# Performance work log

Measured on AMD Instinct MI355X. Metric: run time of the kernel, lower is better.

Reference implementation:

```python
import jax, jax.numpy as jnp
import numpy as np

DIM = 1024
N_HEADS = 16
HEAD_DIM = DIM // N_HEADS
BATCH = 2
SEQ = 2048


def rotate_half(x):
    x1, x2 = jnp.split(x, 2, axis=-1)
    return jnp.concatenate((-x2, x1), axis=-1)


def rope_cos_sin(seq_len, head_dim, dtype=jnp.float32):
    inv_freq = 1.0 / (10000.0 ** (jnp.arange(0, head_dim, 2, dtype=jnp.float32) / head_dim))
    t = jnp.arange(seq_len, dtype=jnp.float32)
    freqs = jnp.einsum('i,j->ij', t, inv_freq)          # [S, hd/2]
    emb = jnp.concatenate((freqs, freqs), axis=-1)       # [S, hd]
    return emb.astype(dtype)[None, :, None, :]           # [1, S, 1, hd] (cos/sin applied below)


def setup_inputs() -> dict:
    key = jax.random.key(0)
    k_x, k_q, k_k, k_v, k_o = jax.random.split(key, 5)
    scale = 1.0 / np.sqrt(DIM)
    x = jax.random.normal(k_x, (BATCH, SEQ, DIM), dtype=jnp.float32)
    Wq = jax.random.normal(k_q, (DIM, DIM), dtype=jnp.float32) * scale
    Wk = jax.random.normal(k_k, (DIM, DIM), dtype=jnp.float32) * scale
    Wv = jax.random.normal(k_v, (DIM, DIM), dtype=jnp.float32) * scale
    Wo = jax.random.normal(k_o, (DIM, DIM), dtype=jnp.float32) * scale
    # causal mask: scores masked where mask == 0
    mask = jnp.tril(jnp.ones((SEQ, SEQ), dtype=jnp.int32))[None, None, :, :]
    return {"x": x, "Wq": Wq, "Wk": Wk, "Wv": Wv, "Wo": Wo, "mask": mask}


def reference(x, Wq, Wk, Wv, Wo, mask):
    B, S, _ = x.shape
    # torch nn.Linear: y = x @ W.T
    q = (x @ Wq.T).reshape(B, S, N_HEADS, HEAD_DIM)
    k = (x @ Wk.T).reshape(B, S, N_HEADS, HEAD_DIM)
    v = (x @ Wv.T).reshape(B, S, N_HEADS, HEAD_DIM)
    ang = rope_cos_sin(S, HEAD_DIM, x.dtype)
    cos, sin = jnp.cos(ang), jnp.sin(ang)
    q = q * cos + rotate_half(q) * sin
    k = k * cos + rotate_half(k) * sin
    # [B, H, S, hd]
    q = q.transpose(0, 2, 1, 3)
    k = k.transpose(0, 2, 1, 3)
    v = v.transpose(0, 2, 1, 3)
    scores = jnp.einsum('bhqd,bhkd->bhqk', q, k) / np.sqrt(HEAD_DIM)
    scores = jnp.where(mask == 0, jnp.asarray(-1e9, scores.dtype), scores)
    attn = jax.nn.softmax(scores, axis=-1)
    out = jnp.einsum('bhqk,bhkd->bhqd', attn, v)
    out = out.transpose(0, 2, 1, 3).reshape(B, S, DIM)
    return out @ Wo.T
```

## Files before the change

### kernel.cpp

```cpp
#include <hip/hip_runtime.h>
#include <stdint.h>

typedef unsigned short u16;
typedef __bf16 bf16x8 __attribute__((ext_vector_type(8)));
typedef __bf16 bf16x4 __attribute__((ext_vector_type(4)));
typedef float f32x4 __attribute__((ext_vector_type(4)));

#define N_B 2
#define N_S 2048
#define N_D 1024
#define N_H 16
#define HD 64

#if __has_builtin(__builtin_amdgcn_exp2f)
#define EXP2F(x) __builtin_amdgcn_exp2f(x)
#else
#define EXP2F(x) exp2f(x)
#endif

__device__ __forceinline__ u16 f2bf(float f) {
  union { float f; uint32_t u; } v; v.f = f;
  uint32_t u = v.u + 0x7fffu + ((v.u >> 16) & 1u);
  return (u16)(u >> 16);
}

__device__ __forceinline__ void gload16(const u16* g, u16* lds) {
  __builtin_amdgcn_global_load_lds(
      (const __attribute__((address_space(1))) unsigned int*)g,
      (__attribute__((address_space(3))) unsigned int*)lds, 16, 0, 0);
}

__global__ __launch_bounds__(256) void prep_kernel(
    const float* __restrict__ x, const float* __restrict__ Wq,
    const float* __restrict__ Wk, const float* __restrict__ Wv,
    const float* __restrict__ Wo,
    u16* __restrict__ xb, u16* __restrict__ wqb, u16* __restrict__ wkb,
    u16* __restrict__ wvb, u16* __restrict__ wob,
    float* __restrict__ cosT, float* __restrict__ sinT)
{
  const int NX = N_B * N_S * N_D;
  const int NW = N_D * N_D;
  int bid = blockIdx.x;
  if (bid < 8192) {
    int i = (bid * 256 + threadIdx.x) * 4;
    const float* src; u16* dst; int off;
    if (i < NX) { src = x; dst = xb; off = i; }
    else {
      int j = i - NX;
      int w = j >> 20;
      off = j & (NW - 1);
      src = (w == 0) ? Wq : (w == 1) ? Wk : (w == 2) ? Wv : Wo;
      dst = (w == 0) ? wqb : (w == 1) ? wkb : (w == 2) ? wvb : wob;
    }
    float4 v = *(const float4*)(src + off);
    ushort4 o;
    o.x = f2bf(v.x); o.y = f2bf(v.y); o.z = f2bf(v.z); o.w = f2bf(v.w);
    *(ushort4*)(dst + off) = o;
  } else {
    int t = (bid - 8192) * 256 + threadIdx.x;
    int s = t >> 5, i = t & 31;
    float inv = expf(-(float)i * 0.28782313662425574f);
    float a = (float)s * inv;
    float sn, cs;
    sincosf(a, &sn, &cs);
    cosT[t] = cs;
    sinT[t] = sn;
  }
}

__global__ __launch_bounds__(256, 5) void proj_kernel(
    const u16* __restrict__ x, const u16* __restrict__ Wq,
    const u16* __restrict__ Wk, const u16* __restrict__ Wv,
    u16* __restrict__ Qb, u16* __restrict__ Kb, u16* __restrict__ Vtb,
    const float* __restrict__ cosT, const float* __restrict__ sinT)
{
  const int mode = blockIdx.z;
  const u16* Wm = (mode == 0) ? Wq : (mode == 1) ? Wk : Wv;
  const int bx = blockIdx.x, by = blockIdx.y;
  const int tid = threadIdx.x;
  const int wave = tid >> 6, lane = tid & 63;
  const int c = lane & 15, quad = lane >> 4;

  __shared__ __align__(16) u16 As[128 * 64];
  __shared__ __align__(16) u16 Bs[64 * 64];

  const f32x4 zero = {0.f, 0.f, 0.f, 0.f};
  f32x4 acc[2][4];
#pragma unroll
  for (int i = 0; i < 2; ++i)
#pragma unroll
    for (int j = 0; j < 4; ++j) acc[i][j] = zero;

  for (int kt = 0; kt < 16; ++kt) {
    const int k0 = kt * 64;
    __syncthreads();
#pragma unroll
    for (int t = 0; t < 4; ++t) {
      int p = t * 256 + tid;
      int m = p >> 3, sl = p & 7;
      int kq = sl ^ (m & 7);
      gload16(x + (size_t)(by * 128 + m) * N_D + k0 + kq * 8, &As[(t * 256 + wave * 64) * 8]);
    }
#pragma unroll
    for (int t = 0; t < 2; ++t) {
      int p = t * 256 + tid;
      int m = p >> 3, sl = p & 7;
      int kq = sl ^ (m & 7);
      gload16(Wm + (size_t)(bx * 64 + m) * N_D + k0 + kq * 8, &Bs[(t * 256 + wave * 64) * 8]);
    }
    __syncthreads();
#pragma unroll
    for (int ks = 0; ks < 2; ++ks) {
      bf16x8 av[2], bv[4];
      int kq = ks * 4 + quad;
#pragma unroll
      for (int i = 0; i < 2; ++i) {
        int m = wave * 32 + i * 16 + c;
        av[i] = *(const bf16x8*)&As[(m * 8 + (kq ^ (m & 7))) * 8];
      }
#pragma unroll
      for (int j = 0; j < 4; ++j) {
        int n = j * 16 + c;
        bv[j] = *(const bf16x8*)&Bs[(n * 8 + (kq ^ (n & 7))) * 8];
      }
#pragma unroll
      for (int i = 0; i < 2; ++i)
#pragma unroll
        for (int j = 0; j < 4; ++j)
          acc[i][j] = __builtin_amdgcn_mfma_f32_16x16x32_bf16(av[i], bv[j], acc[i][j], 0, 0, 0);
    }
  }

  const int h = bx;
  if (mode < 2) {
    u16* Out = (mode == 0) ? Qb : Kb;
#pragma unroll
    for (int i = 0; i < 2; ++i) {
#pragma unroll
      for (int r = 0; r < 4; ++r) {
        int row = by * 128 + wave * 32 + i * 16 + quad * 4 + r;
        int b = row >> 11, s = row & 2047;
        float cs0 = cosT[s * 32 + c],      sn0 = sinT[s * 32 + c];
        float cs1 = cosT[s * 32 + 16 + c], sn1 = sinT[s * 32 + 16 + c];
        size_t base = ((size_t)(b * N_H + h) * N_S + s) * HD;
#pragma unroll
        for (int j = 0; j < 4; ++j) {
          float v = acc[i][j][r];
          float p = acc[i][j ^ 2][r];
          float cs = (j & 1) ? cs1 : cs0;
          float sn = (j & 1) ? sn1 : sn0;
          float res = (j < 2) ? (v * cs - p * sn) : (v * cs + p * sn);
          Out[base + j * 16 + c] = f2bf(res);
        }
      }
    }
  } else {
#pragma unroll
    for (int i = 0; i < 2; ++i) {
      int srow = by * 128 + wave * 32 + i * 16 + quad * 4;
      int b = srow >> 11, sb = srow & 2047;
#pragma unroll
      for (int j = 0; j < 4; ++j) {
        int d = j * 16 + c;
        ushort4 pk;
        pk.x = f2bf(acc[i][j][0]);
        pk.y = f2bf(acc[i][j][1]);
        pk.z = f2bf(acc[i][j][2]);
        pk.w = f2bf(acc[i][j][3]);
        *(ushort4*)&Vtb[((size_t)(b * N_H + h) * HD + d) * N_S + sb] = pk;
      }
    }
  }
}

__global__ __launch_bounds__(64, 2) void attn_kernel(
    const u16* __restrict__ Qb, const u16* __restrict__ Kb,
    const u16* __restrict__ Vtb, u16* __restrict__ Ab)
{
  const int lane = threadIdx.x;
  const int c = lane & 15, quad = lane >> 4;
  const int bx = blockIdx.x;
  const int xcd = bx & 7;
  const int idx = bx >> 3;
  const int t = 63 - (idx >> 2);
  const int bh = xcd + (idx & 3) * 8;
  const int q0 = t * 32;
  const int ktmax = t >> 1;
  const int maskch = t & 1;

  __shared__ __align__(16) u16 Ks[2][64 * 64];
  __shared__ __align__(16) u16 Ps[32 * 32];

  const u16* Qg = Qb + ((size_t)bh * N_S + q0) * HD;
  const u16* Kg = Kb + (size_t)bh * N_S * HD;
  const u16* Vg = Vtb + (size_t)bh * HD * N_S;

  bf16x8 qreg[2][2];
#pragma unroll
  for (int jQ = 0; jQ < 2; ++jQ)
#pragma unroll
    for (int ks = 0; ks < 2; ++ks)
      qreg[jQ][ks] = *(const bf16x8*)(Qg + (jQ * 16 + c) * HD + ks * 32 + quad * 8);

  const f32x4 zero = {0.f, 0.f, 0.f, 0.f};
  f32x4 acc_o[2][4];
#pragma unroll
  for (int mt = 0; mt < 2; ++mt)
#pragma unroll
    for (int nt = 0; nt < 4; ++nt) acc_o[mt][nt] = zero;
  float lrow[2] = {0.f, 0.f};

  const float CLOG = 0.18033688011112042f;
  const float FM = 16.0f;

#pragma unroll
  for (int i = 0; i < 8; ++i) {
    int ci = i * 64 + lane;
    int m = ci >> 3, sl = ci & 7;
    int kq = sl ^ (m & 7);
    gload16(Kg + (size_t)m * HD + kq * 8, &Ks[0][i * 512]);
  }
  asm volatile("" ::: "memory");
  bf16x8 vf[2][4];
#pragma unroll
  for (int ch = 0; ch < 2; ++ch)
#pragma unroll
    for (int nt = 0; nt < 4; ++nt)
      vf[ch][nt] = *(const bf16x8*)(Vg + (size_t)(nt * 16 + c) * N_S + ch * 32 + quad * 8);

  for (int kt = 0; kt <= ktmax; ++kt) {
    const u16* kb = &Ks[kt & 1][0];
    if (kt < ktmax) {
#pragma unroll
      for (int i = 0; i < 8; ++i) {
        int ci = i * 64 + lane;
        int m = ci >> 3, sl = ci & 7;
        int kq = sl ^ (m & 7);
        gload16(Kg + (size_t)((kt + 1) * 64 + m) * HD + kq * 8, &Ks[(kt + 1) & 1][i * 512]);
      }
      asm volatile("s_waitcnt vmcnt(16)" ::: "memory");
    } else {
      asm volatile("s_waitcnt vmcnt(8)" ::: "memory");
    }

    const bool diag = (kt == ktmax);
    const int nch = (diag && maskch == 0) ? 1 : 2;

#pragma unroll
    for (int ch = 0; ch < 2; ++ch) {
      if (ch < nch) {
        f32x4 acc_s[2][2];
#pragma unroll
        for (int iK = 0; iK < 2; ++iK)
#pragma unroll
          for (int jQ = 0; jQ < 2; ++jQ) acc_s[iK][jQ] = zero;
#pragma unroll
        for (int ks = 0; ks < 2; ++ks) {
          bf16x8 kf[2];
          int kq = ks * 4 + quad;
#pragma unroll
          for (int iK = 0; iK < 2; ++iK) {
            int m = ch * 32 + iK * 16 + c;
            kf[iK] = *(const bf16x8*)&kb[(m * 8 + (kq ^ (m & 7))) * 8];
          }
#pragma unroll
          for (int iK = 0; iK < 2; ++iK)
#pragma unroll
            for (int jQ = 0; jQ < 2; ++jQ)
              acc_s[iK][jQ] = __builtin_amdgcn_mfma_f32_16x16x32_bf16(
                  kf[iK], qreg[jQ][ks], acc_s[iK][jQ], 0, 0, 0);
        }

        const bool domask = diag && (ch == maskch);
#pragma unroll
        for (int iK = 0; iK < 2; ++iK)
#pragma unroll
          for (int jQ = 0; jQ < 2; ++jQ) {
            bf16x4 pb;
#pragma unroll
            for (int rr = 0; rr < 4; ++rr) {
              float arg = fmaf(acc_s[iK][jQ][rr], CLOG, -FM);
              if (domask) {
                int dsk = iK * 16 + quad * 4 + rr;
                int dq = jQ * 16 + c;
                if (dsk > dq) arg = -3.0e38f;
              }
              float p = EXP2F(arg);
              lrow[jQ] += p;
              pb[rr] = (__bf16)p;
            }
            int q = jQ * 16 + c;
            int slot = (iK * 2 + (quad >> 1)) ^ (q & 3);
            *(bf16x4*)&Ps[q * 32 + slot * 8 + (quad & 1) * 4] = pb;
          }

        bf16x8 pf[2];
#pragma unroll
        for (int mt = 0; mt < 2; ++mt) {
          int q = mt * 16 + c;
          pf[mt] = *(const bf16x8*)&Ps[q * 32 + ((quad ^ (q & 3)) * 8)];
        }
#pragma unroll
        for (int mt = 0; mt < 2; ++mt)
#pragma unroll
          for (int nt = 0; nt < 4; ++nt)
            acc_o[mt][nt] = __builtin_amdgcn_mfma_f32_16x16x32_bf16(
                pf[mt], vf[ch][nt], acc_o[mt][nt], 0, 0, 0);
      }
    }

    if (kt < ktmax) {
#pragma unroll
      for (int ch = 0; ch < 2; ++ch)
#pragma unroll
        for (int nt = 0; nt < 4; ++nt)
          vf[ch][nt] = *(const bf16x8*)(Vg + (size_t)(nt * 16 + c) * N_S
                                        + (kt + 1) * 64 + ch * 32 + quad * 8);
    }
  }

#pragma unroll
  for (int jQ = 0; jQ < 2; ++jQ) {
    float l = lrow[jQ];
    l += __shfl_xor(l, 16, 64);
    l += __shfl_xor(l, 32, 64);
    lrow[jQ] = 1.0f / l;
  }
  const int b = bh >> 4, h = bh & 15;
#pragma unroll
  for (int mt = 0; mt < 2; ++mt) {
#pragma unroll
    for (int rr = 0; rr < 4; ++rr) {
      float inv = __shfl(lrow[mt], quad * 4 + rr, 64);
      int q = q0 + mt * 16 + quad * 4 + rr;
#pragma unroll
      for (int nt = 0; nt < 4; ++nt) {
        Ab[((size_t)(b * N_S + q)) * N_D + h * HD + nt * 16 + c] =
            f2bf(acc_o[mt][nt][rr] * inv);
      }
    }
  }
}

__global__ __launch_bounds__(256) void out_gemm_kernel(
    const u16* __restrict__ A, const u16* __restrict__ Wo, float* __restrict__ out)
{
  const int bx = blockIdx.x, by = blockIdx.y;
  const int tid = threadIdx.x;
  const int wave = tid >> 6, lane = tid & 63;
  const int c = lane & 15, quad = lane >> 4;
  const int wm = wave & 1, wn = wave >> 1;

  __shared__ __align__(16) u16 As[64 * 64];
  __shared__ __align__(16) u16 Bs[64 * 64];

  const f32x4 zero = {0.f, 0.f, 0.f, 0.f};
  f32x4 acc[2][2];
#pragma unroll
  for (int i = 0; i < 2; ++i)
#pragma unroll
    for (int j = 0; j < 2; ++j) acc[i][j] = zero;

  for (int kt = 0; kt < 16; ++kt) {
    const int k0 = kt * 64;
    __syncthreads();
#pragma unroll
    for (int t = 0; t < 2; ++t) {
      int p = t * 256 + tid;
      int m = p >> 3, sl = p & 7;
      int kq = sl ^ (m & 7);
      gload16(A + (size_t)(by * 64 + m) * N_D + k0 + kq * 8, &As[(t * 256 + wave * 64) * 8]);
    }
#pragma unroll
    for (int t = 0; t < 2; ++t) {
      int p = t * 256 + tid;
      int m = p >> 3, sl = p & 7;
      int kq = sl ^ (m & 7);
      gload16(Wo + (size_t)(bx * 64 + m) * N_D + k0 + kq * 8, &Bs[(t * 256 + wave * 64) * 8]);
    }
    __syncthreads();
#pragma unroll
    for (int ks = 0; ks < 2; ++ks) {
      bf16x8 av[2], bv[2];
      int kq = ks * 4 + quad;
#pragma unroll
      for (int i = 0; i < 2; ++i) {
        int m = wm * 32 + i * 16 + c;
        av[i] = *(const bf16x8*)&As[(m * 8 + (kq ^ (m & 7))) * 8];
      }
#pragma unroll
      for (int j = 0; j < 2; ++j) {
        int n = wn * 32 + j * 16 + c;
        bv[j] = *(const bf16x8*)&Bs[(n * 8 + (kq ^ (n & 7))) * 8];
      }
#pragma unroll
      for (int i = 0; i < 2; ++i)
#pragma unroll
        for (int j = 0; j < 2; ++j)
          acc[i][j] = __builtin_amdgcn_mfma_f32_16x16x32_bf16(av[i], bv[j], acc[i][j], 0, 0, 0);
    }
  }

#pragma unroll
  for (int i = 0; i < 2; ++i)
#pragma unroll
    for (int r = 0; r < 4; ++r) {
      int row = by * 64 + wm * 32 + i * 16 + quad * 4 + r;
#pragma unroll
      for (int j = 0; j < 2; ++j) {
        int col = bx * 64 + wn * 32 + j * 16 + c;
        out[(size_t)row * N_D + col] = acc[i][j][r];
      }
    }
}

extern "C" void kernel_launch(void* const* d_in, const int* in_sizes, int n_in,
                              void* d_out, int out_size, void* d_ws, size_t ws_size,
                              hipStream_t stream) {
  const float* x  = (const float*)d_in[0];
  const float* Wq = (const float*)d_in[1];
  const float* Wk = (const float*)d_in[2];
  const float* Wv = (const float*)d_in[3];
  const float* Wo = (const float*)d_in[4];
  float* out = (float*)d_out;
  char* ws = (char*)d_ws;
  u16* xb   = (u16*)(ws);
  u16* Wqb  = (u16*)(ws + ( 8u << 20));
  u16* Wkb  = (u16*)(ws + (10u << 20));
  u16* Wvb  = (u16*)(ws + (12u << 20));
  u16* Wob  = (u16*)(ws + (14u << 20));
  u16* Qb   = (u16*)(ws + (16u << 20));
  u16* Kb   = (u16*)(ws + (24u << 20));
  u16* Vtb  = (u16*)(ws + (32u << 20));
  u16* Ab   = (u16*)(ws + (40u << 20));
  float* cosT = (float*)(ws + (48u << 20));
  float* sinT = (float*)(ws + (48u << 20) + (1u << 20));

  prep_kernel<<<8448, 256, 0, stream>>>(x, Wq, Wk, Wv, Wo,
                                        xb, Wqb, Wkb, Wvb, Wob, cosT, sinT);
  proj_kernel<<<dim3(16, 32, 3), 256, 0, stream>>>(xb, Wqb, Wkb, Wvb, Qb, Kb, Vtb, cosT, sinT);
  attn_kernel<<<2048, 64, 0, stream>>>(Qb, Kb, Vtb, Ab);
  out_gemm_kernel<<<dim3(16, 64), 256, 0, stream>>>(Ab, Wob, out);
}
```

Baseline: 206.0 us.

## Split attention KV range across two waves and enlarge output GEMM tiles

The attention kernel now runs two waves per block. Each wave handles half of the key tiles for the same 32 query rows, and the partial outputs and row sums are combined through shared memory at the end. K fragments are now loaded straight from global memory into registers instead of being double-buffered in LDS. The output GEMM tile grows to 128x64 per block, with each wave computing 32x64, which reuses B fragments more at the cost of more registers per thread. These changes aim to shorten the serial per-block KV loop on long causal rows and improve data reuse, but they add a reduction step and lose the LDS sharing of K.

```diff
diff --git a/kernel.cpp b/kernel.cpp
--- a/kernel.cpp
+++ b/kernel.cpp
@@ -173,11 +173,13 @@
   }
 }
 
-__global__ __launch_bounds__(64, 2) void attn_kernel(
+__global__ __launch_bounds__(128, 3) void attn_kernel(
     const u16* __restrict__ Qb, const u16* __restrict__ Kb,
     const u16* __restrict__ Vtb, u16* __restrict__ Ab)
 {
-  const int lane = threadIdx.x;
+  const int tid = threadIdx.x;
+  const int wave = tid >> 6;
+  const int lane = tid & 63;
   const int c = lane & 15, quad = lane >> 4;
   const int bx = blockIdx.x;
   const int xcd = bx & 7;
@@ -185,15 +187,20 @@
   const int t = 63 - (idx >> 2);
   const int bh = xcd + (idx & 3) * 8;
   const int q0 = t * 32;
-  const int ktmax = t >> 1;
+  const int nk = (t >> 1) + 1;
+  const int nk0 = (nk + 1) >> 1;
+  const int kb = wave ? nk0 : 0;
+  const int ke = wave ? nk : nk0;
   const int maskch = t & 1;
 
-  __shared__ __align__(16) u16 Ks[2][64 * 64];
-  __shared__ __align__(16) u16 Ps[32 * 32];
+  __shared__ __align__(16) u16 Ps[2][32 * 32];
+  __shared__ float Os[32][68];
+  __shared__ float Ls[32];
 
   const u16* Qg = Qb + ((size_t)bh * N_S + q0) * HD;
   const u16* Kg = Kb + (size_t)bh * N_S * HD;
   const u16* Vg = Vtb + (size_t)bh * HD * N_S;
+  u16* Psw = &Ps[wave][0];
 
   bf16x8 qreg[2][2];
 #pragma unroll
@@ -213,109 +220,97 @@
   const float CLOG = 0.18033688011112042f;
   const float FM = 16.0f;
 
-#pragma unroll
-  for (int i = 0; i < 8; ++i) {
-    int ci = i * 64 + lane;
-    int m = ci >> 3, sl = ci & 7;
-    int kq = sl ^ (m & 7);
-    gload16(Kg + (size_t)m * HD + kq * 8, &Ks[0][i * 512]);
-  }
-  asm volatile("" ::: "memory");
-  bf16x8 vf[2][4];
-#pragma unroll
-  for (int ch = 0; ch < 2; ++ch)
-#pragma unroll
-    for (int nt = 0; nt < 4; ++nt)
-      vf[ch][nt] = *(const bf16x8*)(Vg + (size_t)(nt * 16 + c) * N_S + ch * 32 + quad * 8);
-
-  for (int kt = 0; kt <= ktmax; ++kt) {
-    const u16* kb = &Ks[kt & 1][0];
-    if (kt < ktmax) {
-#pragma unroll
-      for (int i = 0; i < 8; ++i) {
-        int ci = i * 64 + lane;
-        int m = ci >> 3, sl = ci & 7;
-        int kq = sl ^ (m & 7);
-        gload16(Kg + (size_t)((kt + 1) * 64 + m) * HD + kq * 8, &Ks[(kt + 1) & 1][i * 512]);
-      }
-      asm volatile("s_waitcnt vmcnt(16)" ::: "memory");
-    } else {
-      asm volatile("s_waitcnt vmcnt(8)" ::: "memory");
-    }
-
-    const bool diag = (kt == ktmax);
-    const int nch = (diag && maskch == 0) ? 1 : 2;
-
-#pragma unroll
-    for (int ch = 0; ch < 2; ++ch) {
-      if (ch < nch) {
-        f32x4 acc_s[2][2];
-#pragma unroll
-        for (int iK = 0; iK < 2; ++iK)
-#pragma unroll
-          for (int jQ = 0; jQ < 2; ++jQ) acc_s[iK][jQ] = zero;
-#pragma unroll
-        for (int ks = 0; ks < 2; ++ks) {
-          bf16x8 kf[2];
-          int kq = ks * 4 + quad;
-#pragma unroll
-          for (int iK = 0; iK < 2; ++iK) {
-            int m = ch * 32 + iK * 16 + c;
-            kf[iK] = *(const bf16x8*)&kb[(m * 8 + (kq ^ (m & 7))) * 8];
+#define LOADK(dst, kt_, ch_)                                                  \
+  {                                                                           \
+    _Pragma("unroll") for (int iK = 0; iK < 2; ++iK)                          \
+      _Pragma("unroll") for (int ks = 0; ks < 2; ++ks)                        \
+        dst[iK][ks] = *(const bf16x8*)(Kg +                                   \
+            (size_t)((kt_) * 64 + (ch_) * 32 + iK * 16 + c) * HD +            \
+            ks * 32 + quad * 8);                                              \
+  }
+
+  bf16x8 kA[2][2], kB[2][2], vf[2][4];
+
+  auto chunk = [&](int ch, const bf16x8 (&kf)[2][2], bool domask) {
+    f32x4 acc_s[2][2];
+#pragma unroll
+    for (int iK = 0; iK < 2; ++iK)
+#pragma unroll
+      for (int jQ = 0; jQ < 2; ++jQ) acc_s[iK][jQ] = zero;
+#pragma unroll
+    for (int ks = 0; ks < 2; ++ks)
+#pragma unroll
+      for (int iK = 0; iK < 2; ++iK)
+#pragma unroll
+        for (int jQ = 0; jQ < 2; ++jQ)
+          acc_s[iK][jQ] = __builtin_amdgcn_mfma_f32_16x16x32_bf16(
+              kf[iK][ks], qreg[jQ][ks], acc_s[iK][jQ], 0, 0, 0);
+
+#pragma unroll
+    for (int iK = 0; iK < 2; ++iK)
+#pragma unroll
+      for (int jQ = 0; jQ < 2; ++jQ) {
+        bf16x4 pb;
+#pragma unroll
+        for (int rr = 0; rr < 4; ++rr) {
+          float arg = fmaf(acc_s[iK][jQ][rr], CLOG, -FM);
+          if (domask) {
+            int dsk = iK * 16 + quad * 4 + rr;
+            int dq = jQ * 16 + c;
+            if (dsk > dq) arg = -3.0e38f;
           }
-#pragma unroll
-          for (int iK = 0; iK < 2; ++iK)
-#pragma unroll
-            for (int jQ = 0; jQ < 2; ++jQ)
-              acc_s[iK][jQ] = __builtin_amdgcn_mfma_f32_16x16x32_bf16(
-                  kf[iK], qreg[jQ][ks], acc_s[iK][jQ], 0, 0, 0);
+          float p = EXP2F(arg);
+          lrow[jQ] += p;
+          pb[rr] = (__bf16)p;
         }
-
-        const bool domask = diag && (ch == maskch);
-#pragma unroll
-        for (int iK = 0; iK < 2; ++iK)
-#pragma unroll
-          for (int jQ = 0; jQ < 2; ++jQ) {
-            bf16x4 pb;
-#pragma unroll
-            for (int rr = 0; rr < 4; ++rr) {
-              float arg = fmaf(acc_s[iK][jQ][rr], CLOG, -FM);
-              if (domask) {
-                int dsk = iK * 16 + quad * 4 + rr;
-                int dq = jQ * 16 + c;
-                if (dsk > dq) arg = -3.0e38f;
-              }
-              float p = EXP2F(arg);
-              lrow[jQ] += p;
-              pb[rr] = (__bf16)p;
-            }
-            int q = jQ * 16 + c;
-            int slot = (iK * 2 + (quad >> 1)) ^ (q & 3);
-            *(bf16x4*)&Ps[q * 32 + slot * 8 + (quad & 1) * 4] = pb;
-          }
-
-        bf16x8 pf[2];
-#pragma unroll
-        for (int mt = 0; mt < 2; ++mt) {
-          int q = mt * 16 + c;
-          pf[mt] = *(const bf16x8*)&Ps[q * 32 + ((quad ^ (q & 3)) * 8)];
-        }
-#pragma unroll
-        for (int mt = 0; mt < 2; ++mt)
-#pragma unroll
-          for (int nt = 0; nt < 4; ++nt)
-            acc_o[mt][nt] = __builtin_amdgcn_mfma_f32_16x16x32_bf16(
-                pf[mt], vf[ch][nt], acc_o[mt][nt], 0, 0, 0);
-      }
-    }
-
-    if (kt < ktmax) {
-#pragma unroll
-      for (int ch = 0; ch < 2; ++ch)
+        int q = jQ * 16 + c;
+        int slot = (iK * 2 + (quad >> 1)) ^ (q & 3);
+        *(bf16x4*)&Psw[q * 32 + slot * 8 + (quad & 1) * 4] = pb;
+      }
+
+    bf16x8 pf[2];
+#pragma unroll
+    for (int mt = 0; mt < 2; ++mt) {
+      int q = mt * 16 + c;
+      pf[mt] = *(const bf16x8*)&Psw[q * 32 + ((quad ^ (q & 3)) * 8)];
+    }
+#pragma unroll
+    for (int mt = 0; mt < 2; ++mt)
+#pragma unroll
+      for (int nt = 0; nt < 4; ++nt)
+        acc_o[mt][nt] = __builtin_amdgcn_mfma_f32_16x16x32_bf16(
+            pf[mt], vf[ch][nt], acc_o[mt][nt], 0, 0, 0);
+  };
+
+  if (kb < ke) {
+    LOADK(kA, kb, 0);
+#pragma unroll
+    for (int ch2 = 0; ch2 < 2; ++ch2)
+#pragma unroll
+      for (int nt = 0; nt < 4; ++nt)
+        vf[ch2][nt] = *(const bf16x8*)(Vg + (size_t)(nt * 16 + c) * N_S
+                                       + kb * 64 + ch2 * 32 + quad * 8);
+  }
+
+  for (int kt = kb; kt < ke; ++kt) {
+    const bool diag = (kt == nk - 1);
+    const bool skip1 = diag && (maskch == 0);
+
+    if (!skip1) LOADK(kB, kt, 1);
+    chunk(0, kA, diag && (maskch == 0));
+
+    if (!skip1) {
+      if (kt + 1 < ke) LOADK(kA, kt + 1, 0);
+      chunk(1, kB, diag && (maskch == 1));
+    }
+
+    if (kt + 1 < ke) {
+#pragma unroll
+      for (int ch2 = 0; ch2 < 2; ++ch2)
 #pragma unroll
         for (int nt = 0; nt < 4; ++nt)
-          vf[ch][nt] = *(const bf16x8*)(Vg + (size_t)(nt * 16 + c) * N_S
-                                        + (kt + 1) * 64 + ch * 32 + quad * 8);
+          vf[ch2][nt] = *(const bf16x8*)(Vg + (size_t)(nt * 16 + c) * N_S
+                                         + (kt + 1) * 64 + ch2 * 32 + quad * 8);
     }
   }
 
@@ -324,52 +319,71 @@
     float l = lrow[jQ];
     l += __shfl_xor(l, 16, 64);
     l += __shfl_xor(l, 32, 64);
-    lrow[jQ] = 1.0f / l;
-  }
-  const int b = bh >> 4, h = bh & 15;
-#pragma unroll
-  for (int mt = 0; mt < 2; ++mt) {
-#pragma unroll
-    for (int rr = 0; rr < 4; ++rr) {
-      float inv = __shfl(lrow[mt], quad * 4 + rr, 64);
-      int q = q0 + mt * 16 + quad * 4 + rr;
-#pragma unroll
-      for (int nt = 0; nt < 4; ++nt) {
-        Ab[((size_t)(b * N_S + q)) * N_D + h * HD + nt * 16 + c] =
-            f2bf(acc_o[mt][nt][rr] * inv);
-      }
-    }
-  }
-}
-
-__global__ __launch_bounds__(256) void out_gemm_kernel(
+    lrow[jQ] = l;
+  }
+
+  if (wave == 1) {
+#pragma unroll
+    for (int mt = 0; mt < 2; ++mt)
+#pragma unroll
+      for (int nt = 0; nt < 4; ++nt)
+#pragma unroll
+        for (int rr = 0; rr < 4; ++rr)
+          Os[mt * 16 + quad * 4 + rr][nt * 16 + c] = acc_o[mt][nt][rr];
+    if (quad == 0) { Ls[c] = lrow[0]; Ls[16 + c] = lrow[1]; }
+  }
+  __syncthreads();
+  if (wave == 0) {
+    float inv[2];
+#pragma unroll
+    for (int jQ = 0; jQ < 2; ++jQ)
+      inv[jQ] = 1.0f / (lrow[jQ] + Ls[jQ * 16 + c]);
+    const int b = bh >> 4, h = bh & 15;
+#pragma unroll
+    for (int mt = 0; mt < 2; ++mt) {
+#pragma unroll
+      for (int rr = 0; rr < 4; ++rr) {
+        float iv = __shfl(inv[mt], quad * 4 + rr, 64);
+        int lr = mt * 16 + quad * 4 + rr;
+        int q = q0 + lr;
+#pragma unroll
+        for (int nt = 0; nt < 4; ++nt) {
+          float val = (acc_o[mt][nt][rr] + Os[lr][nt * 16 + c]) * iv;
+          Ab[((size_t)(b * N_S + q)) * N_D + h * HD + nt * 16 + c] = f2bf(val);
+        }
+      }
+    }
+  }
+#undef LOADK
+}
+
+__global__ __launch_bounds__(256, 2) void out_gemm_kernel(
     const u16* __restrict__ A, const u16* __restrict__ Wo, float* __restrict__ out)
 {
   const int bx = blockIdx.x, by = blockIdx.y;
   const int tid = threadIdx.x;
   const int wave = tid >> 6, lane = tid & 63;
   const int c = lane & 15, quad = lane >> 4;
-  const int wm = wave & 1, wn = wave >> 1;
-
-  __shared__ __align__(16) u16 As[64 * 64];
+
+  __shared__ __align__(16) u16 As[128 * 64];
   __shared__ __align__(16) u16 Bs[64 * 64];
 
   const f32x4 zero = {0.f, 0.f, 0.f, 0.f};
-  f32x4 acc[2][2];
+  f32x4 acc[2][4];
 #pragma unroll
   for (int i = 0; i < 2; ++i)
 #pragma unroll
-    for (int j = 0; j < 2; ++j) acc[i][j] = zero;
+    for (int j = 0; j < 4; ++j) acc[i][j] = zero;
 
   for (int kt = 0; kt < 16; ++kt) {
     const int k0 = kt * 64;
     __syncthreads();
 #pragma unroll
-    for (int t = 0; t < 2; ++t) {
+    for (int t = 0; t < 4; ++t) {
       int p = t * 256 + tid;
       int m = p >> 3, sl = p & 7;
       int kq = sl ^ (m & 7);
-      gload16(A + (size_t)(by * 64 + m) * N_D + k0 + kq * 8, &As[(t * 256 + wave * 64) * 8]);
+      gload16(A + (size_t)(by * 128 + m) * N_D + k0 + kq * 8, &As[(t * 256 + wave * 64) * 8]);
     }
 #pragma unroll
     for (int t = 0; t < 2; ++t) {
@@ -381,22 +395,22 @@
     __syncthreads();
 #pragma unroll
     for (int ks = 0; ks < 2; ++ks) {
-      bf16x8 av[2], bv[2];
+      bf16x8 av[2], bv[4];
       int kq = ks * 4 + quad;
 #pragma unroll
       for (int i = 0; i < 2; ++i) {
-        int m = wm * 32 + i * 16 + c;
+        int m = wave * 32 + i * 16 + c;
         av[i] = *(const bf16x8*)&As[(m * 8 + (kq ^ (m & 7))) * 8];
       }
 #pragma unroll
-      for (int j = 0; j < 2; ++j) {
-        int n = wn * 32 + j * 16 + c;
+      for (int j = 0; j < 4; ++j) {
+        int n = j * 16 + c;
         bv[j] = *(const bf16x8*)&Bs[(n * 8 + (kq ^ (n & 7))) * 8];
       }
 #pragma unroll
       for (int i = 0; i < 2; ++i)
 #pragma unroll
-        for (int j = 0; j < 2; ++j)
+        for (int j = 0; j < 4; ++j)
           acc[i][j] = __builtin_amdgcn_mfma_f32_16x16x32_bf16(av[i], bv[j], acc[i][j], 0, 0, 0);
     }
   }
@@ -405,10 +419,10 @@
   for (int i = 0; i < 2; ++i)
 #pragma unroll
     for (int r = 0; r < 4; ++r) {
-      int row = by * 64 + wm * 32 + i * 16 + quad * 4 + r;
-#pragma unroll
-      for (int j = 0; j < 2; ++j) {
-        int col = bx * 64 + wn * 32 + j * 16 + c;
+      int row = by * 128 + wave * 32 + i * 16 + quad * 4 + r;
+#pragma unroll
+      for (int j = 0; j < 4; ++j) {
+        int col = bx * 64 + j * 16 + c;
         out[(size_t)row * N_D + col] = acc[i][j][r];
       }
     }
@@ -439,6 +453,6 @@
   prep_kernel<<<8448, 256, 0, stream>>>(x, Wq, Wk, Wv, Wo,
                                         xb, Wqb, Wkb, Wvb, Wob, cosT, sinT);
   proj_kernel<<<dim3(16, 32, 3), 256, 0, stream>>>(xb, Wqb, Wkb, Wvb, Qb, Kb, Vtb, cosT, sinT);
-  attn_kernel<<<2048, 64, 0, stream>>>(Qb, Kb, Vtb, Ab);
-  out_gemm_kernel<<<dim3(16, 64), 256, 0, stream>>>(Ab, Wob, out);
-}
+  attn_kernel<<<2048, 128, 0, stream>>>(Qb, Kb, Vtb, Ab);
+  out_gemm_kernel<<<dim3(16, 32), 256, 0, stream>>>(Ab, Wob, out);
+}
```

Measured after the change: 224.9 us. 1.09x slower.
